# Performance work log

Measured on AMD Instinct MI355X. Metric: run time of the kernel, lower is better.

Reference implementation:

```python
import jax, jax.numpy as jnp
import numpy as np

N_NODES = 100000
N_EDGES = 3200000
F_IN, HID, N_CLS = 256, 16, 40


def gcn_conv(x, row, col, W, b, n):
    """PyG GCNConv: x@W, symmetric deg^-1/2 normalization with self-loops, scatter-add to targets."""
    xw = x @ W  # [N, out]
    deg = jax.ops.segment_sum(jnp.ones_like(col, dtype=xw.dtype), col, num_segments=n)
    dinv = jnp.where(deg > 0, jax.lax.rsqrt(deg), jnp.zeros_like(deg))
    norm = dinv[row] * dinv[col]  # [E+N]
    out = jax.ops.segment_sum(norm[:, None] * xw[row], col, num_segments=n)
    return out + b


def setup_inputs() -> dict:
    key = jax.random.key(0)
    k1, k2, k3, k4 = jax.random.split(key, 4)
    x = jax.random.normal(k1, (N_NODES, F_IN), dtype=jnp.float32)
    edge_index = jax.random.randint(k2, (2, N_EDGES), 0, N_NODES, dtype=jnp.int64)
    W1 = jax.random.normal(k3, (F_IN, HID), dtype=jnp.float32) / np.sqrt(F_IN)
    b1 = jnp.zeros((HID,), dtype=jnp.float32)
    W2 = jax.random.normal(k4, (HID, N_CLS), dtype=jnp.float32) / np.sqrt(HID)
    b2 = jnp.zeros((N_CLS,), dtype=jnp.float32)
    return {"x": x, "edge_index": edge_index, "W1": W1, "b1": b1, "W2": W2, "b2": b2}


def reference(x, edge_index, W1, b1, W2, b2):
    n = x.shape[0]
    loop = jnp.arange(n, dtype=edge_index.dtype)
    row = jnp.concatenate([edge_index[0], loop])  # sources (+ self-loops)
    col = jnp.concatenate([edge_index[1], loop])  # targets (+ self-loops)
    h = gcn_conv(x, row, col, W1, b1, n)
    h = jax.nn.relu(h)
    # dropout p=0.5 is identity in eval mode (self.training == False)
    h = gcn_conv(h, row, col, W2, b2, n)
    return jax.nn.log_softmax(h, axis=1)
```

## Files before the change

kernel.cpp:

```cpp
#include <hip/hip_runtime.h>

#define F_IN 256
#define HID  16
#define NCLS 40
#define NB   512
#define CAP  18944
#define SPAN 4096

static inline int cdiv(int a, int b) { return (a + b - 1) / b; }

typedef short bf16x8 __attribute__((ext_vector_type(8)));
typedef float f32x4  __attribute__((ext_vector_type(4)));

__device__ __forceinline__ float bf_lo(unsigned int u) { return __uint_as_float(u << 16); }
__device__ __forceinline__ float bf_hi(unsigned int u) { return __uint_as_float(u & 0xFFFF0000u); }
__device__ __forceinline__ unsigned short f2bf(float a) {
    unsigned int u = __float_as_uint(a);
    return (unsigned short)((u + 0x7FFFu + ((u >> 16) & 1u)) >> 16);
}
__device__ __forceinline__ unsigned int pack_bf(float a, float b) {
    return (unsigned int)f2bf(a) | ((unsigned int)f2bf(b) << 16);
}

__global__ void __launch_bounds__(256) bcount_kernel(const int* __restrict__ col,
                                                     int* __restrict__ bkt_cnt, int E, int K) {
    __shared__ int h[256];
    int t = threadIdx.x;
    h[t] = 0;
    __syncthreads();
    int E4 = E >> 2;
    const int4* c4 = (const int4*)col;
    for (int e = blockIdx.x * 256 + t; e < E4; e += gridDim.x * 256) {
        int4 v = c4[e];
        atomicAdd(&h[v.x >> 9], 1);
        atomicAdd(&h[v.y >> 9], 1);
        atomicAdd(&h[v.z >> 9], 1);
        atomicAdd(&h[v.w >> 9], 1);
    }
    for (int e = (E4 << 2) + blockIdx.x * 256 + t; e < E; e += gridDim.x * 256)
        atomicAdd(&h[col[e] >> 9], 1);
    __syncthreads();
    if (t < K && h[t]) atomicAdd(&bkt_cnt[t], h[t]);
}

__global__ void __launch_bounds__(256) bscan_kernel(const int* __restrict__ bkt_cnt,
                                                    int* __restrict__ bkt_off,
                                                    int* __restrict__ bkt_cur, int K) {
    __shared__ int s[256];
    int t = threadIdx.x;
    int v = (t < K) ? bkt_cnt[t] : 0;
    s[t] = v;
    __syncthreads();
    for (int off = 1; off < 256; off <<= 1) {
        int x = (t >= off) ? s[t - off] : 0;
        __syncthreads();
        s[t] += x;
        __syncthreads();
    }
    int excl = s[t] - v;
    if (t < K) { bkt_off[t] = excl; bkt_cur[t] = excl; }
    if (t == K - 1) bkt_off[K] = excl + v;
}

__global__ void __launch_bounds__(256) bscatter_kernel(const int* __restrict__ row,
                                                       const int* __restrict__ col,
                                                       int* __restrict__ bkt_cur,
                                                       int* __restrict__ entries, int E) {
    __shared__ int cnt[256];
    __shared__ int base[256];
    int t = threadIdx.x;
    int start = blockIdx.x * SPAN;
    int end = min(start + SPAN, E);
    cnt[t] = 0;
    __syncthreads();
    int m = end - start;
    int m4 = m >> 2;
    const int4* c4 = (const int4*)(col + start);
    for (int i = t; i < m4; i += 256) {
        int4 v = c4[i];
        atomicAdd(&cnt[v.x >> 9], 1);
        atomicAdd(&cnt[v.y >> 9], 1);
        atomicAdd(&cnt[v.z >> 9], 1);
        atomicAdd(&cnt[v.w >> 9], 1);
    }
    for (int i = (m4 << 2) + t; i < m; i += 256)
        atomicAdd(&cnt[col[start + i] >> 9], 1);
    __syncthreads();
    int c = cnt[t];
    base[t] = c ? atomicAdd(&bkt_cur[t], c) : 0;
    cnt[t] = 0;
    __syncthreads();
    int e = start + t;
    for (; e + 1792 < end; e += 2048) {
        int c0 = col[e];
        int c1 = col[e + 256];
        int c2 = col[e + 512];
        int c3 = col[e + 768];
        int c4v = col[e + 1024];
        int c5 = col[e + 1280];
        int c6 = col[e + 1536];
        int c7 = col[e + 1792];
        int r0 = row[e];
        int r1 = row[e + 256];
        int r2 = row[e + 512];
        int r3 = row[e + 768];
        int r4 = row[e + 1024];
        int r5 = row[e + 1280];
        int r6 = row[e + 1536];
        int r7 = row[e + 1792];
        int b0 = c0 >> 9, b1 = c1 >> 9, b2 = c2 >> 9, b3 = c3 >> 9;
        int b4 = c4v >> 9, b5 = c5 >> 9, b6 = c6 >> 9, b7 = c7 >> 9;
        int p0 = base[b0] + atomicAdd(&cnt[b0], 1);
        int p1 = base[b1] + atomicAdd(&cnt[b1], 1);
        int p2 = base[b2] + atomicAdd(&cnt[b2], 1);
        int p3 = base[b3] + atomicAdd(&cnt[b3], 1);
        int p4 = base[b4] + atomicAdd(&cnt[b4], 1);
        int p5 = base[b5] + atomicAdd(&cnt[b5], 1);
        int p6 = base[b6] + atomicAdd(&cnt[b6], 1);
        int p7 = base[b7] + atomicAdd(&cnt[b7], 1);
        entries[p0] = r0 | ((c0 & (NB - 1)) << 17);
        entries[p1] = r1 | ((c1 & (NB - 1)) << 17);
        entries[p2] = r2 | ((c2 & (NB - 1)) << 17);
        entries[p3] = r3 | ((c3 & (NB - 1)) << 17);
        entries[p4] = r4 | ((c4v & (NB - 1)) << 17);
        entries[p5] = r5 | ((c5 & (NB - 1)) << 17);
        entries[p6] = r6 | ((c6 & (NB - 1)) << 17);
        entries[p7] = r7 | ((c7 & (NB - 1)) << 17);
    }
    for (; e < end; e += 256) {
        int cc = col[e];
        int bkt = cc >> 9;
        int pos = base[bkt] + atomicAdd(&cnt[bkt], 1);
        entries[pos] = row[e] | ((cc & (NB - 1)) << 17);
    }
}

__global__ void __launch_bounds__(512) bfill_kernel(const int* __restrict__ entries,
                                                    const int* __restrict__ bkt_off,
                                                    int* __restrict__ csr_src,
                                                    int* __restrict__ csr_off,
                                                    float* __restrict__ dinv, int n, int E) {
    __shared__ int sdeg[NB];
    __shared__ int soff[NB];
    __shared__ int wtot[8];
    __shared__ int lsrc[CAP];
    int t = threadIdx.x;
    int wv = t >> 6, ln = t & 63;
    int b = blockIdx.x;
    int node0 = b << 9;
    int nn = min(NB, n - node0);
    int seg0 = bkt_off[b], seg1 = bkt_off[b + 1];
    int m = seg1 - seg0;
    sdeg[t] = 0;
    __syncthreads();
    {
        int i = t;
        for (; i + 1536 < m; i += 2048) {
            int u0 = entries[seg0 + i];
            int u1 = entries[seg0 + i + 512];
            int u2 = entries[seg0 + i + 1024];
            int u3 = entries[seg0 + i + 1536];
            atomicAdd(&sdeg[u0 >> 17], 1);
            atomicAdd(&sdeg[u1 >> 17], 1);
            atomicAdd(&sdeg[u2 >> 17], 1);
            atomicAdd(&sdeg[u3 >> 17], 1);
        }
        for (; i < m; i += 512) atomicAdd(&sdeg[entries[seg0 + i] >> 17], 1);
    }
    __syncthreads();
    int v = sdeg[t];
    int inc = v;
#pragma unroll
    for (int o = 1; o < 64; o <<= 1) {
        int u = __shfl_up(inc, o);
        if (ln >= o) inc += u;
    }
    if (ln == 63) wtot[wv] = inc;
    __syncthreads();
    if (wv == 0) {
        int tv = (ln < 8) ? wtot[ln] : 0;
        int ti = tv;
#pragma unroll
        for (int o = 1; o < 8; o <<= 1) {
            int u = __shfl_up(ti, o);
            if (ln >= o) ti += u;
        }
        if (ln < 8) wtot[ln] = ti - tv;
    }
    __syncthreads();
    int excl = inc - v + wtot[wv];
    sdeg[t] = 0;
    soff[t] = excl;
    __syncthreads();
    {
        int i = t;
        for (; i + 1536 < m; i += 2048) {
            int u0 = entries[seg0 + i];
            int u1 = entries[seg0 + i + 512];
            int u2 = entries[seg0 + i + 1024];
            int u3 = entries[seg0 + i + 1536];
            int l0 = u0 >> 17, l1 = u1 >> 17, l2 = u2 >> 17, l3 = u3 >> 17;
            int p0 = soff[l0] + atomicAdd(&sdeg[l0], 1);
            int p1 = soff[l1] + atomicAdd(&sdeg[l1], 1);
            int p2 = soff[l2] + atomicAdd(&sdeg[l2], 1);
            int p3 = soff[l3] + atomicAdd(&sdeg[l3], 1);
            lsrc[p0] = u0 & 0x1FFFF;
            lsrc[p1] = u1 & 0x1FFFF;
            lsrc[p2] = u2 & 0x1FFFF;
            lsrc[p3] = u3 & 0x1FFFF;
        }
        for (; i < m; i += 512) {
            int u = entries[seg0 + i];
            int l = u >> 17;
            int pos = soff[l] + atomicAdd(&sdeg[l], 1);
            lsrc[pos] = u & 0x1FFFF;
        }
    }
    __syncthreads();
    for (int i = t; i < m; i += 512) csr_src[seg0 + i] = lsrc[i];
    if (t < nn) {
        csr_off[node0 + t] = seg0 + excl;
        dinv[node0 + t] = rsqrtf((float)(v + 1));
    }
    if (b == gridDim.x - 1 && t == 0) csr_off[n] = E;
}

__global__ void __launch_bounds__(256) xw_kernel(const float* __restrict__ x,
                                                 const float* __restrict__ W1,
                                                 const float* __restrict__ dinv,
                                                 unsigned short* __restrict__ f1,
                                                 int ntiles) {
    int lane = threadIdx.x & 63;
    int m = lane & 15;
    int q = lane >> 4;
    bf16x8 bfrag[8];
#pragma unroll
    for (int c = 0; c < 8; ++c) {
        const float* wp = W1 + (size_t)(c * 32 + q * 8) * HID + m;
#pragma unroll
        for (int j = 0; j < 8; ++j) bfrag[c][j] = (short)f2bf(wp[(size_t)j * HID]);
    }
    int wid = (blockIdx.x * 256 + threadIdx.x) >> 6;
    if (wid >= ntiles) return;
    int r0 = wid << 4;
    const float* xrow = x + (size_t)(r0 + m) * F_IN + q * 8;
    f32x4 acc = {0.f, 0.f, 0.f, 0.f};
#pragma unroll
    for (int c = 0; c < 8; ++c) {
        float4 v0 = *(const float4*)(xrow + c * 32);
        float4 v1 = *(const float4*)(xrow + c * 32 + 4);
        bf16x8 afrag;
        afrag[0] = (short)f2bf(v0.x);
        afrag[1] = (short)f2bf(v0.y);
        afrag[2] = (short)f2bf(v0.z);
        afrag[3] = (short)f2bf(v0.w);
        afrag[4] = (short)f2bf(v1.x);
        afrag[5] = (short)f2bf(v1.y);
        afrag[6] = (short)f2bf(v1.z);
        afrag[7] = (short)f2bf(v1.w);
        acc = __builtin_amdgcn_mfma_f32_16x16x32_bf16(afrag, bfrag[c], acc, 0, 0, 0);
    }
#pragma unroll
    for (int i = 0; i < 4; ++i) {
        int r = r0 + q * 4 + i;
        f1[(size_t)r * HID + m] = f2bf(dinv[r] * acc[i]);
    }
}

__global__ void __launch_bounds__(1024) agg1_kernel(const uint2* __restrict__ feat2,
                                                    const float* __restrict__ dinv,
                                                    const int* __restrict__ csr_off,
                                                    const int* __restrict__ csr_src,
                                                    const float* __restrict__ b1,
                                                    uint2* __restrict__ f2, int n) {
    int wid = (blockIdx.x * 1024 + threadIdx.x) >> 6;
    int w0 = wid << 1;
    if (w0 >= n) return;
    int lane = threadIdx.x & 63;
    int j = lane & 3;
    int s = (lane >> 2) & 7;
    int node = w0 + (lane >> 5);
    bool act = node < n;
    int start = 0, end = 0;
    if (act) { start = csr_off[node]; end = csr_off[node + 1]; }
    bool sl = act && (s == 0);
    uint2 us = feat2[(size_t)(act ? node : 0) * 4 + j];
    float a0 = 0.f, a1 = 0.f, a2 = 0.f, a3 = 0.f;
    if (act && start < end) {
        int e = start + s;
        bool v0 = e      < end, v1 = e + 8  < end, v2 = e + 16 < end, v3 = e + 24 < end;
        bool v4 = e + 32 < end, v5 = e + 40 < end, v6 = e + 48 < end, v7 = e + 56 < end;
        int i0 = csr_src[v0 ? e      : start];
        int i1 = csr_src[v1 ? e + 8  : start];
        int i2 = csr_src[v2 ? e + 16 : start];
        int i3 = csr_src[v3 ? e + 24 : start];
        int i4 = csr_src[v4 ? e + 32 : start];
        int i5 = csr_src[v5 ? e + 40 : start];
        int i6 = csr_src[v6 ? e + 48 : start];
        int i7 = csr_src[v7 ? e + 56 : start];
        uint2 u0 = feat2[(size_t)i0 * 4 + j];
        uint2 u1 = feat2[(size_t)i1 * 4 + j];
        uint2 u2 = feat2[(size_t)i2 * 4 + j];
        uint2 u3 = feat2[(size_t)i3 * 4 + j];
        uint2 u4 = feat2[(size_t)i4 * 4 + j];
        uint2 u5 = feat2[(size_t)i5 * 4 + j];
        uint2 u6 = feat2[(size_t)i6 * 4 + j];
        uint2 u7 = feat2[(size_t)i7 * 4 + j];
        if (!v0) { u0.x = 0u; u0.y = 0u; }
        if (!v1) { u1.x = 0u; u1.y = 0u; }
        if (!v2) { u2.x = 0u; u2.y = 0u; }
        if (!v3) { u3.x = 0u; u3.y = 0u; }
        if (!v4) { u4.x = 0u; u4.y = 0u; }
        if (!v5) { u5.x = 0u; u5.y = 0u; }
        if (!v6) { u6.x = 0u; u6.y = 0u; }
        if (!v7) { u7.x = 0u; u7.y = 0u; }
        a0 += bf_lo(u0.x); a1 += bf_hi(u0.x); a2 += bf_lo(u0.y); a3 += bf_hi(u0.y);
        a0 += bf_lo(u1.x); a1 += bf_hi(u1.x); a2 += bf_lo(u1.y); a3 += bf_hi(u1.y);
        a0 += bf_lo(u2.x); a1 += bf_hi(u2.x); a2 += bf_lo(u2.y); a3 += bf_hi(u2.y);
        a0 += bf_lo(u3.x); a1 += bf_hi(u3.x); a2 += bf_lo(u3.y); a3 += bf_hi(u3.y);
        a0 += bf_lo(u4.x); a1 += bf_hi(u4.x); a2 += bf_lo(u4.y); a3 += bf_hi(u4.y);
        a0 += bf_lo(u5.x); a1 += bf_hi(u5.x); a2 += bf_lo(u5.y); a3 += bf_hi(u5.y);
        a0 += bf_lo(u6.x); a1 += bf_hi(u6.x); a2 += bf_lo(u6.y); a3 += bf_hi(u6.y);
        a0 += bf_lo(u7.x); a1 += bf_hi(u7.x); a2 += bf_lo(u7.y); a3 += bf_hi(u7.y);
        for (int e2 = e + 64; e2 < end; e2 += 8) {
            uint2 u = feat2[(size_t)csr_src[e2] * 4 + j];
            a0 += bf_lo(u.x); a1 += bf_hi(u.x); a2 += bf_lo(u.y); a3 += bf_hi(u.y);
        }
    }
    if (sl) {
        a0 += bf_lo(us.x); a1 += bf_hi(us.x); a2 += bf_lo(us.y); a3 += bf_hi(us.y);
    }
    a0 += __shfl_xor(a0, 4);  a1 += __shfl_xor(a1, 4);  a2 += __shfl_xor(a2, 4);  a3 += __shfl_xor(a3, 4);
    a0 += __shfl_xor(a0, 8);  a1 += __shfl_xor(a1, 8);  a2 += __shfl_xor(a2, 8);  a3 += __shfl_xor(a3, 8);
    a0 += __shfl_xor(a0, 16); a1 += __shfl_xor(a1, 16); a2 += __shfl_xor(a2, 16); a3 += __shfl_xor(a3, 16);
    if ((lane & 31) < 4 && act) {
        float dc = dinv[node];
        float4 bb = *(const float4*)(b1 + 4 * j);
        float v0 = fmaxf(dc * a0 + bb.x, 0.f);
        float v1 = fmaxf(dc * a1 + bb.y, 0.f);
        float v2 = fmaxf(dc * a2 + bb.z, 0.f);
        float v3 = fmaxf(dc * a3 + bb.w, 0.f);
        uint2 o;
        o.x = pack_bf(dc * v0, dc * v1);
        o.y = pack_bf(dc * v2, dc * v3);
        f2[(size_t)node * 4 + j] = o;
    }
}

__global__ void __launch_bounds__(1024) agg2out_kernel(const uint2* __restrict__ feat2,
                                                       const float* __restrict__ dinv,
                                                       const int* __restrict__ csr_off,
                                                       const int* __restrict__ csr_src,
                                                       const float* __restrict__ W2,
                                                       const float* __restrict__ b2,
                                                       float* __restrict__ out, int n) {
    __shared__ float W2s[HID * NCLS];
    __shared__ float b2s[NCLS];
    for (int i = threadIdx.x; i < HID * NCLS; i += 1024) W2s[i] = W2[i];
    if (threadIdx.x < NCLS) b2s[threadIdx.x] = b2[threadIdx.x];
    __syncthreads();
    int wid = (blockIdx.x * 1024 + threadIdx.x) >> 6;
    int w0 = wid << 1;
    if (w0 >= n) return;
    int lane = threadIdx.x & 63;
    int j = lane & 3;
    int s = (lane >> 2) & 7;
    int node = w0 + (lane >> 5);
    bool act = node < n;
    int start = 0, end = 0;
    if (act) { start = csr_off[node]; end = csr_off[node + 1]; }
    bool sl = act && (s == 0);
    uint2 us = feat2[(size_t)(act ? node : 0) * 4 + j];
    float a0 = 0.f, a1 = 0.f, a2 = 0.f, a3 = 0.f;
    if (act && start < end) {
        int e = start + s;
        bool v0 = e      < end, v1 = e + 8  < end, v2 = e + 16 < end, v3 = e + 24 < end;
        bool v4 = e + 32 < end, v5 = e + 40 < end, v6 = e + 48 < end, v7 = e + 56 < end;
        int i0 = csr_src[v0 ? e      : start];
        int i1 = csr_src[v1 ? e + 8  : start];
        int i2 = csr_src[v2 ? e + 16 : start];
        int i3 = csr_src[v3 ? e + 24 : start];
        int i4 = csr_src[v4 ? e + 32 : start];
        int i5 = csr_src[v5 ? e + 40 : start];
        int i6 = csr_src[v6 ? e + 48 : start];
        int i7 = csr_src[v7 ? e + 56 : start];
        uint2 u0 = feat2[(size_t)i0 * 4 + j];
        uint2 u1 = feat2[(size_t)i1 * 4 + j];
        uint2 u2 = feat2[(size_t)i2 * 4 + j];
        uint2 u3 = feat2[(size_t)i3 * 4 + j];
        uint2 u4 = feat2[(size_t)i4 * 4 + j];
        uint2 u5 = feat2[(size_t)i5 * 4 + j];
        uint2 u6 = feat2[(size_t)i6 * 4 + j];
        uint2 u7 = feat2[(size_t)i7 * 4 + j];
        if (!v0) { u0.x = 0u; u0.y = 0u; }
        if (!v1) { u1.x = 0u; u1.y = 0u; }
        if (!v2) { u2.x = 0u; u2.y = 0u; }
        if (!v3) { u3.x = 0u; u3.y = 0u; }
        if (!v4) { u4.x = 0u; u4.y = 0u; }
        if (!v5) { u5.x = 0u; u5.y = 0u; }
        if (!v6) { u6.x = 0u; u6.y = 0u; }
        if (!v7) { u7.x = 0u; u7.y = 0u; }
        a0 += bf_lo(u0.x); a1 += bf_hi(u0.x); a2 += bf_lo(u0.y); a3 += bf_hi(u0.y);
        a0 += bf_lo(u1.x); a1 += bf_hi(u1.x); a2 += bf_lo(u1.y); a3 += bf_hi(u1.y);
        a0 += bf_lo(u2.x); a1 += bf_hi(u2.x); a2 += bf_lo(u2.y); a3 += bf_hi(u2.y);
        a0 += bf_lo(u3.x); a1 += bf_hi(u3.x); a2 += bf_lo(u3.y); a3 += bf_hi(u3.y);
        a0 += bf_lo(u4.x); a1 += bf_hi(u4.x); a2 += bf_lo(u4.y); a3 += bf_hi(u4.y);
        a0 += bf_lo(u5.x); a1 += bf_hi(u5.x); a2 += bf_lo(u5.y); a3 += bf_hi(u5.y);
        a0 += bf_lo(u6.x); a1 += bf_hi(u6.x); a2 += bf_lo(u6.y); a3 += bf_hi(u6.y);
        a0 += bf_lo(u7.x); a1 += bf_hi(u7.x); a2 += bf_lo(u7.y); a3 += bf_hi(u7.y);
        for (int e2 = e + 64; e2 < end; e2 += 8) {
            uint2 u = feat2[(size_t)csr_src[e2] * 4 + j];
            a0 += bf_lo(u.x); a1 += bf_hi(u.x); a2 += bf_lo(u.y); a3 += bf_hi(u.y);
        }
    }
    if (sl) {
        a0 += bf_lo(us.x); a1 += bf_hi(us.x); a2 += bf_lo(us.y); a3 += bf_hi(us.y);
    }
    a0 += __shfl_xor(a0, 4);  a1 += __shfl_xor(a1, 4);  a2 += __shfl_xor(a2, 4);  a3 += __shfl_xor(a3, 4);
    a0 += __shfl_xor(a0, 8);  a1 += __shfl_xor(a1, 8);  a2 += __shfl_xor(a2, 8);  a3 += __shfl_xor(a3, 8);
    a0 += __shfl_xor(a0, 16); a1 += __shfl_xor(a1, 16); a2 += __shfl_xor(a2, 16); a3 += __shfl_xor(a3, 16);
    bool hasB = (w0 + 1) < n;
    float dcA = dinv[w0];
    float dcB = hasB ? dinv[w0 + 1] : 0.f;
    float zA = (lane < NCLS) ? b2s[lane] : 0.f;
    float zB = zA;
#pragma unroll
    for (int q = 0; q < 4; ++q) {
        float fA0 = dcA * __shfl(a0, q);
        float fA1 = dcA * __shfl(a1, q);
        float fA2 = dcA * __shfl(a2, q);
        float fA3 = dcA * __shfl(a3, q);
        float fB0 = dcB * __shfl(a0, 32 + q);
        float fB1 = dcB * __shfl(a1, 32 + q);
        float fB2 = dcB * __shfl(a2, 32 + q);
        float fB3 = dcB * __shfl(a3, 32 + q);
        if (lane < NCLS) {
            float w0v = W2s[(4 * q)     * NCLS + lane];
            float w1v = W2s[(4 * q + 1) * NCLS + lane];
            float w2v = W2s[(4 * q + 2) * NCLS + lane];
            float w3v = W2s[(4 * q + 3) * NCLS + lane];
            zA += fA0 * w0v + fA1 * w1v + fA2 * w2v + fA3 * w3v;
            zB += fB0 * w0v + fB1 * w1v + fB2 * w2v + fB3 * w3v;
        }
    }
    float mA = (lane < NCLS) ? zA : -INFINITY;
    float mB = (lane < NCLS) ? zB : -INFINITY;
#pragma unroll
    for (int off = 1; off < 64; off <<= 1) {
        mA = fmaxf(mA, __shfl_xor(mA, off));
        mB = fmaxf(mB, __shfl_xor(mB, off));
    }
    float eA = (lane < NCLS) ? __expf(zA - mA) : 0.f;
    float eB = (lane < NCLS) ? __expf(zB - mB) : 0.f;
#pragma unroll
    for (int off = 1; off < 64; off <<= 1) {
        eA += __shfl_xor(eA, off);
        eB += __shfl_xor(eB, off);
    }
    float lseA = mA + __logf(eA);
    float lseB = mB + __logf(eB);
    if (lane < NCLS) {
        out[(size_t)w0 * NCLS + lane] = zA - lseA;
        if (hasB) out[(size_t)(w0 + 1) * NCLS + lane] = zB - lseB;
    }
}

extern "C" void kernel_launch(void* const* d_in, const int* in_sizes, int n_in,
                              void* d_out, int out_size, void* d_ws, size_t ws_size,
                              hipStream_t stream) {
    const float* x   = (const float*)d_in[0];
    const int*   ei  = (const int*)d_in[1];
    const float* W1  = (const float*)d_in[2];
    const float* b1  = (const float*)d_in[3];
    const float* W2  = (const float*)d_in[4];
    const float* b2  = (const float*)d_in[5];
    float*       out = (float*)d_out;

    int n = in_sizes[0] / F_IN;
    int E = in_sizes[1] / 2;
    const int* rowp = ei;
    const int* colp = ei + E;
    int K = cdiv(n, NB);

    char* p = (char*)d_ws;
    auto alloc = [&](size_t bytes) {
        char* q = p;
        p += (bytes + 255) & ~(size_t)255;
        return q;
    };
    int*   bkt_cnt = (int*)  alloc((size_t)K * 4);
    int*   bkt_off = (int*)  alloc(((size_t)K + 1) * 4);
    int*   bkt_cur = (int*)  alloc((size_t)K * 4);
    int*   csr_off = (int*)  alloc(((size_t)n + 1) * 4);
    int*   csr_src = (int*)  alloc((size_t)E * 4);
    float* dinv    = (float*)alloc((size_t)n * 4);
    size_t fbytes = (size_t)n * HID * 2;
    char* region = alloc((size_t)E * 4 > 2 * fbytes ? (size_t)E * 4 : 2 * fbytes);
    int*            entries = (int*)region;
    unsigned short* f1      = (unsigned short*)region;
    uint2*          f2      = (uint2*)(region + fbytes);

    hipMemsetAsync(bkt_cnt, 0, (size_t)K * 4, stream);
    bcount_kernel<<<1024, 256, 0, stream>>>(colp, bkt_cnt, E, K);
    bscan_kernel<<<1, 256, 0, stream>>>(bkt_cnt, bkt_off, bkt_cur, K);
    bscatter_kernel<<<cdiv(E, SPAN), 256, 0, stream>>>(rowp, colp, bkt_cur, entries, E);
    bfill_kernel<<<K, 512, 0, stream>>>(entries, bkt_off, csr_src, csr_off, dinv, n, E);

    int ntiles = n >> 4;
    xw_kernel<<<cdiv(ntiles, 4), 256, 0, stream>>>(x, W1, dinv, f1, ntiles);
    int npair = cdiv(n, 2);
    agg1_kernel<<<cdiv(npair, 16), 1024, 0, stream>>>((const uint2*)f1, dinv, csr_off, csr_src, b1, f2, n);
    agg2out_kernel<<<cdiv(npair, 16), 1024, 0, stream>>>((const uint2*)f2, dinv, csr_off, csr_src, W2, b2, out, n);
}
```

Measured before the change: 333.1 us.

## Fold bucket scan into scatter and fill kernels; shrink aggregation blocks to 256

Removes the single-block bucket scan launch. The prefix sum over the per-bucket counts is now recomputed redundantly inside every bscatter and bfill block, and bkt_cur becomes a relative cursor that is zeroed by one combined memset. Separately, both aggregation kernels switch from 1024-thread to 256-thread blocks with a matching grid size. This saves one launch and its serialization gap, at the cost of a small redundant scan per block and extra barriers in bfill.

```diff
diff --git a/kernel.cpp b/kernel.cpp
--- a/kernel.cpp
+++ b/kernel.cpp
@@ -43,32 +43,25 @@
     if (t < K && h[t]) atomicAdd(&bkt_cnt[t], h[t]);
 }
 
-__global__ void __launch_bounds__(256) bscan_kernel(const int* __restrict__ bkt_cnt,
-                                                    int* __restrict__ bkt_off,
-                                                    int* __restrict__ bkt_cur, int K) {
-    __shared__ int s[256];
-    int t = threadIdx.x;
-    int v = (t < K) ? bkt_cnt[t] : 0;
-    s[t] = v;
-    __syncthreads();
-    for (int off = 1; off < 256; off <<= 1) {
-        int x = (t >= off) ? s[t - off] : 0;
-        __syncthreads();
-        s[t] += x;
-        __syncthreads();
-    }
-    int excl = s[t] - v;
-    if (t < K) { bkt_off[t] = excl; bkt_cur[t] = excl; }
-    if (t == K - 1) bkt_off[K] = excl + v;
-}
-
 __global__ void __launch_bounds__(256) bscatter_kernel(const int* __restrict__ row,
                                                        const int* __restrict__ col,
+                                                       const int* __restrict__ bkt_cnt,
                                                        int* __restrict__ bkt_cur,
-                                                       int* __restrict__ entries, int E) {
+                                                       int* __restrict__ entries, int E, int K) {
+    __shared__ int scn[256];
     __shared__ int cnt[256];
     __shared__ int base[256];
     int t = threadIdx.x;
+    int gv = (t < K) ? bkt_cnt[t] : 0;
+    scn[t] = gv;
+    __syncthreads();
+    for (int off = 1; off < 256; off <<= 1) {
+        int x = (t >= off) ? scn[t - off] : 0;
+        __syncthreads();
+        scn[t] += x;
+        __syncthreads();
+    }
+    int bkt_base = scn[t] - gv;
     int start = blockIdx.x * SPAN;
     int end = min(start + SPAN, E);
     cnt[t] = 0;
@@ -87,7 +80,7 @@
         atomicAdd(&cnt[col[start + i] >> 9], 1);
     __syncthreads();
     int c = cnt[t];
-    base[t] = c ? atomicAdd(&bkt_cur[t], c) : 0;
+    base[t] = bkt_base + (c ? atomicAdd(&bkt_cur[t], c) : 0);
     cnt[t] = 0;
     __syncthreads();
     int e = start + t;
@@ -136,20 +129,36 @@
 }
 
 __global__ void __launch_bounds__(512) bfill_kernel(const int* __restrict__ entries,
-                                                    const int* __restrict__ bkt_off,
+                                                    const int* __restrict__ bkt_cnt,
                                                     int* __restrict__ csr_src,
                                                     int* __restrict__ csr_off,
-                                                    float* __restrict__ dinv, int n, int E) {
+                                                    float* __restrict__ dinv, int n, int E, int K) {
     __shared__ int sdeg[NB];
     __shared__ int soff[NB];
     __shared__ int wtot[8];
+    __shared__ int gscn[256];
     __shared__ int lsrc[CAP];
     int t = threadIdx.x;
     int wv = t >> 6, ln = t & 63;
     int b = blockIdx.x;
+    if (t < 256) {
+        int gv = (t < K) ? bkt_cnt[t] : 0;
+        gscn[t] = gv;
+    }
+    __syncthreads();
+    if (t < 256) {
+    }
+    for (int off = 1; off < 256; off <<= 1) {
+        int x = 0;
+        if (t < 256 && t >= off) x = gscn[t - off];
+        __syncthreads();
+        if (t < 256) gscn[t] += x;
+        __syncthreads();
+    }
+    int seg0 = (b > 0) ? gscn[b - 1] : 0;
+    int seg1 = gscn[b];
     int node0 = b << 9;
     int nn = min(NB, n - node0);
-    int seg0 = bkt_off[b], seg1 = bkt_off[b + 1];
     int m = seg1 - seg0;
     sdeg[t] = 0;
     __syncthreads();
@@ -267,13 +276,13 @@
     }
 }
 
-__global__ void __launch_bounds__(1024) agg1_kernel(const uint2* __restrict__ feat2,
-                                                    const float* __restrict__ dinv,
-                                                    const int* __restrict__ csr_off,
-                                                    const int* __restrict__ csr_src,
-                                                    const float* __restrict__ b1,
-                                                    uint2* __restrict__ f2, int n) {
-    int wid = (blockIdx.x * 1024 + threadIdx.x) >> 6;
+__global__ void __launch_bounds__(256) agg1_kernel(const uint2* __restrict__ feat2,
+                                                   const float* __restrict__ dinv,
+                                                   const int* __restrict__ csr_off,
+                                                   const int* __restrict__ csr_src,
+                                                   const float* __restrict__ b1,
+                                                   uint2* __restrict__ f2, int n) {
+    int wid = (blockIdx.x * 256 + threadIdx.x) >> 6;
     int w0 = wid << 1;
     if (w0 >= n) return;
     int lane = threadIdx.x & 63;
@@ -347,19 +356,19 @@
     }
 }
 
-__global__ void __launch_bounds__(1024) agg2out_kernel(const uint2* __restrict__ feat2,
-                                                       const float* __restrict__ dinv,
-                                                       const int* __restrict__ csr_off,
-                                                       const int* __restrict__ csr_src,
-                                                       const float* __restrict__ W2,
-                                                       const float* __restrict__ b2,
-                                                       float* __restrict__ out, int n) {
+__global__ void __launch_bounds__(256) agg2out_kernel(const uint2* __restrict__ feat2,
+                                                      const float* __restrict__ dinv,
+                                                      const int* __restrict__ csr_off,
+                                                      const int* __restrict__ csr_src,
+                                                      const float* __restrict__ W2,
+                                                      const float* __restrict__ b2,
+                                                      float* __restrict__ out, int n) {
     __shared__ float W2s[HID * NCLS];
     __shared__ float b2s[NCLS];
-    for (int i = threadIdx.x; i < HID * NCLS; i += 1024) W2s[i] = W2[i];
+    for (int i = threadIdx.x; i < HID * NCLS; i += 256) W2s[i] = W2[i];
     if (threadIdx.x < NCLS) b2s[threadIdx.x] = b2[threadIdx.x];
     __syncthreads();
-    int wid = (blockIdx.x * 1024 + threadIdx.x) >> 6;
+    int wid = (blockIdx.x * 256 + threadIdx.x) >> 6;
     int w0 = wid << 1;
     if (w0 >= n) return;
     int lane = threadIdx.x & 63;
@@ -488,9 +497,9 @@
         p += (bytes + 255) & ~(size_t)255;
         return q;
     };
-    int*   bkt_cnt = (int*)  alloc((size_t)K * 4);
-    int*   bkt_off = (int*)  alloc(((size_t)K + 1) * 4);
-    int*   bkt_cur = (int*)  alloc((size_t)K * 4);
+    int*   bkt_pair = (int*)  alloc((size_t)(2 * 256) * 4);
+    int*   bkt_cnt  = bkt_pair;
+    int*   bkt_cur  = bkt_pair + 256;
     int*   csr_off = (int*)  alloc(((size_t)n + 1) * 4);
     int*   csr_src = (int*)  alloc((size_t)E * 4);
     float* dinv    = (float*)alloc((size_t)n * 4);
@@ -500,15 +509,14 @@
     unsigned short* f1      = (unsigned short*)region;
     uint2*          f2      = (uint2*)(region + fbytes);
 
-    hipMemsetAsync(bkt_cnt, 0, (size_t)K * 4, stream);
+    hipMemsetAsync(bkt_pair, 0, (size_t)(2 * 256) * 4, stream);
     bcount_kernel<<<1024, 256, 0, stream>>>(colp, bkt_cnt, E, K);
-    bscan_kernel<<<1, 256, 0, stream>>>(bkt_cnt, bkt_off, bkt_cur, K);
-    bscatter_kernel<<<cdiv(E, SPAN), 256, 0, stream>>>(rowp, colp, bkt_cur, entries, E);
-    bfill_kernel<<<K, 512, 0, stream>>>(entries, bkt_off, csr_src, csr_off, dinv, n, E);
+    bscatter_kernel<<<cdiv(E, SPAN), 256, 0, stream>>>(rowp, colp, bkt_cnt, bkt_cur, entries, E, K);
+    bfill_kernel<<<K, 512, 0, stream>>>(entries, bkt_cnt, csr_src, csr_off, dinv, n, E, K);
 
     int ntiles = n >> 4;
     xw_kernel<<<cdiv(ntiles, 4), 256, 0, stream>>>(x, W1, dinv, f1, ntiles);
     int npair = cdiv(n, 2);
-    agg1_kernel<<<cdiv(npair, 16), 1024, 0, stream>>>((const uint2*)f1, dinv, csr_off, csr_src, b1, f2, n);
-    agg2out_kernel<<<cdiv(npair, 16), 1024, 0, stream>>>((const uint2*)f2, dinv, csr_off, csr_src, W2, b2, out, n);
-}
+    agg1_kernel<<<cdiv(npair, 4), 256, 0, stream>>>((const uint2*)f1, dinv, csr_off, csr_src, b1, f2, n);
+    agg2out_kernel<<<cdiv(npair, 4), 256, 0, stream>>>((const uint2*)f2, dinv, csr_off, csr_src, W2, b2, out, n);
+}
```

After: 327.4 us. Within noise of the previous version (-1.7%).
